# Kernel tuning notes

Measured on AMD Instinct MI355X. Metric: run time of the kernel, lower is better.

Reference implementation:

```python
import jax, jax.numpy as jnp
import numpy as np

N_NODES = 128   # input_series_dim (nodes per graph)
FEAT = 512      # input_series_length
HID = 512       # hidden_channels
OUT = 10        # output_dimension
BATCH = 512     # batch_size


def setup_inputs() -> dict:
    key = jax.random.key(0)
    ks = jax.random.split(key, 9)
    s = 0.02
    x = jax.random.normal(ks[0], (BATCH, N_NODES, FEAT), jnp.float32)
    # dense_to_sparse(ones(N_NODES, N_NODES)) -> fully connected incl. diagonal,
    # row-major order, covering only nodes 0..N_NODES-1 (faithful to source).
    r = jnp.repeat(jnp.arange(N_NODES, dtype=jnp.int32), N_NODES)
    c = jnp.tile(jnp.arange(N_NODES, dtype=jnp.int32), N_NODES)
    edge_index = jnp.stack([r, c])  # (2, N_NODES**2)
    batch = jnp.repeat(jnp.arange(BATCH, dtype=jnp.int32), N_NODES)  # (BATCH*N_NODES,)
    W1 = jax.random.normal(ks[1], (FEAT, HID), jnp.float32) * s
    b1 = jnp.zeros((HID,), jnp.float32)
    W2 = jax.random.normal(ks[2], (HID, HID), jnp.float32) * s
    b2 = jnp.zeros((HID,), jnp.float32)
    W3 = jax.random.normal(ks[3], (HID, HID), jnp.float32) * s
    b3 = jnp.zeros((HID,), jnp.float32)
    Wlin = jax.random.normal(ks[4], (HID, OUT), jnp.float32) * s
    blin = jnp.zeros((OUT,), jnp.float32)
    return {"x": x, "W1": W1, "b1": b1, "W2": W2, "b2": b2, "W3": W3,
            "b3": b3, "Wlin": Wlin, "blin": blin,
            "edge_index": edge_index, "batch": batch}


def gcn_conv(h, src, dst, W, b):
    # PyG GCNConv: linear transform, add self-loops for ALL N nodes, symmetric norm,
    # scatter-add aggregate at dst, add bias.
    N = h.shape[0]
    h = h @ W
    loop = jnp.arange(N, dtype=src.dtype)
    s = jnp.concatenate([src, loop])
    d = jnp.concatenate([dst, loop])
    deg = jax.ops.segment_sum(jnp.ones(s.shape[0], h.dtype), d, num_segments=N)
    dinv = jnp.where(deg > 0, jax.lax.rsqrt(deg), jnp.zeros((), h.dtype))
    norm = dinv[s] * dinv[d]                     # (E+N,)
    out = jax.ops.segment_sum(norm[:, None] * h[s], d, num_segments=N)
    return out + b


def reference(x, W1, b1, W2, b2, W3, b3, Wlin, blin, edge_index, batch):
    x = x.reshape(-1, x.shape[-1]).astype(jnp.float32)   # (B*N_NODES, FEAT)
    src, dst = edge_index[0], edge_index[1]
    h = jax.nn.relu(gcn_conv(x, src, dst, W1, b1))
    h = jax.nn.relu(gcn_conv(h, src, dst, W2, b2))
    h = gcn_conv(h, src, dst, W3, b3)                    # layers == 3 path
    B = BATCH
    sums = jax.ops.segment_sum(h, batch, num_segments=B)
    cnt = jax.ops.segment_sum(jnp.ones((h.shape[0],), h.dtype), batch, num_segments=B)
    pooled = sums / cnt[:, None]                         # global_mean_pool
    # dropout p=0.5 is identity in eval mode
    return pooled @ Wlin + blin                          # (BATCH, OUT)
```

## Files before the change

### kernel.cpp

```cpp
#include <hip/hip_runtime.h>
#include <hip/hip_bf16.h>


typedef __attribute__((ext_vector_type(8))) short short8;
typedef __attribute__((ext_vector_type(4))) float f32x4;
typedef __attribute__((ext_vector_type(2))) unsigned int uint2v;
typedef __attribute__((ext_vector_type(4))) unsigned int uint4v;

#define AS_G __attribute__((address_space(1)))
#define AS_L __attribute__((address_space(3)))

__device__ __forceinline__ void gload_lds16(const void* g, void* l) {
  __builtin_amdgcn_global_load_lds((const AS_G void*)g, (AS_L void*)l, 16, 0, 0);
}

__device__ __forceinline__ unsigned int pack2_bf16(float a, float b) {
  unsigned int ua = __float_as_uint(a);
  unsigned int ub = __float_as_uint(b);
  ua += 0x7FFFu + ((ua >> 16) & 1u);
  ub += 0x7FFFu + ((ub >> 16) & 1u);
  return (ua >> 16) | (ub & 0xFFFF0000u);
}

__device__ __forceinline__ unsigned short bf16_rne(float a) {
  unsigned int ua = __float_as_uint(a);
  ua += 0x7FFFu + ((ua >> 16) & 1u);
  return (unsigned short)(ua >> 16);
}

__global__ __launch_bounds__(512, 4) void gemm1(
    const float* __restrict__ x,
    const __hip_bfloat16* __restrict__ W1t,
    const float* __restrict__ b1,
    unsigned short* __restrict__ H1)
{
  __shared__ __align__(16) __hip_bfloat16 smem[26368];

  const int t    = threadIdx.x;
  const int orig = blockIdx.x;
  const int wgid = (orig & 7) * 128 + (orig >> 3);
  const int g    = wgid >> 1;
  const int nb   = wgid & 1;

  const int wave = t >> 6;
  const int l    = t & 63;
  const int q    = l >> 4;
  const int r16  = l & 15;
  const int wm   = (wave & 1) * 64;
  const int wn   = (wave >> 1) * 64;

  const int arow = t >> 2;
  const int cc   = t & 3;
  const float* gx = x + ((size_t)g * 128 + arow) * 512 + cc * 8;
  const int awoff = arow * 32 + ((cc ^ ((arow >> 1) & 3)) << 3);

  const int nrow0 = t >> 2;
  const int nrow1 = (512 + t) >> 2;
  const int slot  = t & 3;
  const __hip_bfloat16* gb0 = W1t + (size_t)(nb * 256 + nrow0) * 512 +
                              ((slot ^ ((nrow0 >> 1) & 3)) << 3);
  const __hip_bfloat16* gb1 = W1t + (size_t)(nb * 256 + nrow1) * 512 +
                              ((slot ^ ((nrow1 >> 1) & 3)) << 3);

  f32x4 acc[4][4];
#pragma unroll
  for (int i = 0; i < 4; ++i)
#pragma unroll
    for (int j = 0; j < 4; ++j)
      acc[i][j] = (f32x4)0.0f;

  {
    f32x4 a0 = *(const f32x4*)(const void*)gx;
    f32x4 a1 = *(const f32x4*)(const void*)(gx + 4);
    gload_lds16(gb0, smem + 8192 + wave * 512);
    gload_lds16(gb1, smem + 8192 + 4096 + wave * 512);
    uint4v w;
    w[0] = pack2_bf16(a0[0], a0[1]);
    w[1] = pack2_bf16(a0[2], a0[3]);
    w[2] = pack2_bf16(a1[0], a1[1]);
    w[3] = pack2_bf16(a1[2], a1[3]);
    *(uint4v*)(void*)(smem + awoff) = w;
  }

  for (int kt = 0; kt < 16; ++kt) {
    const int cur = kt & 1;
    const int nxt = cur ^ 1;
    __syncthreads();

    f32x4 aN0, aN1;
    if (kt < 15) {
      const int ko = (kt + 1) * 32;
      aN0 = *(const f32x4*)(const void*)(gx + ko);
      aN1 = *(const f32x4*)(const void*)(gx + ko + 4);
      gload_lds16(gb0 + ko, smem + 8192 + nxt * 8192 + wave * 512);
      gload_lds16(gb1 + ko, smem + 8192 + nxt * 8192 + 4096 + wave * 512);
    }

    short8 af[4], bfr[4];
#pragma unroll
    for (int i = 0; i < 4; ++i) {
      const int row = wm + i * 16 + r16;
      const int c   = (q ^ ((row >> 1) & 3)) << 3;
      af[i] = *(const short8*)(const void*)(smem + cur * 4096 + row * 32 + c);
    }
#pragma unroll
    for (int j = 0; j < 4; ++j) {
      const int row = wn + j * 16 + r16;
      const int c   = (q ^ ((row >> 1) & 3)) << 3;
      bfr[j] = *(const short8*)(const void*)(smem + 8192 + cur * 8192 + row * 32 + c);
    }
    __builtin_amdgcn_s_setprio(1);
#pragma unroll
    for (int i = 0; i < 4; ++i)
#pragma unroll
      for (int j = 0; j < 4; ++j)
        acc[i][j] = __builtin_amdgcn_mfma_f32_16x16x32_bf16(af[i], bfr[j], acc[i][j], 0, 0, 0);
    __builtin_amdgcn_s_setprio(0);

    if (kt < 15) {
      uint4v w;
      w[0] = pack2_bf16(aN0[0], aN0[1]);
      w[1] = pack2_bf16(aN0[2], aN0[3]);
      w[2] = pack2_bf16(aN1[0], aN1[1]);
      w[3] = pack2_bf16(aN1[2], aN1[3]);
      *(uint4v*)(void*)(smem + nxt * 4096 + awoff) = w;
    }
  }

  float* redf = (float*)(smem + 24576);
  float* Sbuf = (float*)(smem + 25600);

  if (g == 0) {
    float sj[4];
#pragma unroll
    for (int j = 0; j < 4; ++j) {
      float a = 0.0f;
#pragma unroll
      for (int i = 0; i < 4; ++i)
#pragma unroll
        for (int r = 0; r < 4; ++r)
          a += acc[i][j][r];
      a += __shfl_xor(a, 16, 64);
      a += __shfl_xor(a, 32, 64);
      sj[j] = a;
    }
    __syncthreads();
    if (q == 0) {
#pragma unroll
      for (int j = 0; j < 4; ++j) redf[wave * 64 + j * 16 + r16] = sj[j];
    }
    __syncthreads();
    if (t < 256)
      Sbuf[t] = redf[(2 * (t >> 6)) * 64 + (t & 63)] +
                redf[(2 * (t >> 6) + 1) * 64 + (t & 63)];
    __syncthreads();
#pragma unroll
    for (int j = 0; j < 4; ++j) {
      const int col = wn + j * 16 + r16;
      const float bv = b1[nb * 256 + col];
      const float Sv = Sbuf[col];
#pragma unroll
      for (int i = 0; i < 4; ++i)
#pragma unroll
        for (int r = 0; r < 4; ++r) {
          const int row = wm + i * 16 + q * 4 + r;
          const float v = fmaxf((Sv + acc[i][j][r]) * (1.0f / 129.0f) + bv, 0.0f);
          const float o = __shfl_xor(v, 1, 64);
          if ((r16 & 1) == 0)
            *(unsigned int*)(void*)(H1 + (size_t)(g * 128 + row) * 512 + nb * 256 + col) =
                pack2_bf16(v, o);
        }
    }
  } else {
#pragma unroll
    for (int j = 0; j < 4; ++j) {
      const int col = wn + j * 16 + r16;
      const float bv = b1[nb * 256 + col];
#pragma unroll
      for (int i = 0; i < 4; ++i)
#pragma unroll
        for (int r = 0; r < 4; ++r) {
          const int row = wm + i * 16 + q * 4 + r;
          const float v = fmaxf(acc[i][j][r] + bv, 0.0f);
          const float o = __shfl_xor(v, 1, 64);
          if ((r16 & 1) == 0)
            *(unsigned int*)(void*)(H1 + (size_t)(g * 128 + row) * 512 + nb * 256 + col) =
                pack2_bf16(v, o);
        }
    }
  }
}

__global__ __launch_bounds__(512, 4) void gemm2(
    const unsigned short* __restrict__ H1,
    const __hip_bfloat16* __restrict__ W2t,
    const float* __restrict__ b2,
    float* __restrict__ P)
{
  __shared__ __align__(16) __hip_bfloat16 smem[26368];

  const int t    = threadIdx.x;
  const int orig = blockIdx.x;
  const int wgid = (orig & 7) * 128 + (orig >> 3);
  const int g    = wgid >> 1;
  const int nb   = wgid & 1;

  const int wave = t >> 6;
  const int l    = t & 63;
  const int q    = l >> 4;
  const int r16  = l & 15;
  const int wm   = (wave & 1) * 64;
  const int wn   = (wave >> 1) * 64;

  const int arow = t >> 2;
  const int slot = t & 3;
  const unsigned short* gaA = H1 + (size_t)(g * 128 + arow) * 512 +
                              ((slot ^ ((arow >> 1) & 3)) << 3);
  const int nrow0 = t >> 2;
  const int nrow1 = (512 + t) >> 2;
  const __hip_bfloat16* gb0 = W2t + (size_t)(nb * 256 + nrow0) * 512 +
                              ((slot ^ ((nrow0 >> 1) & 3)) << 3);
  const __hip_bfloat16* gb1 = W2t + (size_t)(nb * 256 + nrow1) * 512 +
                              ((slot ^ ((nrow1 >> 1) & 3)) << 3);

  f32x4 acc[4][4];
#pragma unroll
  for (int i = 0; i < 4; ++i)
#pragma unroll
    for (int j = 0; j < 4; ++j)
      acc[i][j] = (f32x4)0.0f;

  gload_lds16(gaA, smem + wave * 512);
  gload_lds16(gb0, smem + 8192 + wave * 512);
  gload_lds16(gb1, smem + 8192 + 4096 + wave * 512);

  for (int kt = 0; kt < 16; ++kt) {
    const int cur = kt & 1;
    const int nxt = cur ^ 1;
    __syncthreads();

    if (kt < 15) {
      const int ko = (kt + 1) * 32;
      gload_lds16(gaA + ko, smem + nxt * 4096 + wave * 512);
      gload_lds16(gb0 + ko, smem + 8192 + nxt * 8192 + wave * 512);
      gload_lds16(gb1 + ko, smem + 8192 + nxt * 8192 + 4096 + wave * 512);
    }

    short8 af[4], bfr[4];
#pragma unroll
    for (int i = 0; i < 4; ++i) {
      const int row = wm + i * 16 + r16;
      const int c   = (q ^ ((row >> 1) & 3)) << 3;
      af[i] = *(const short8*)(const void*)(smem + cur * 4096 + row * 32 + c);
    }
#pragma unroll
    for (int j = 0; j < 4; ++j) {
      const int row = wn + j * 16 + r16;
      const int c   = (q ^ ((row >> 1) & 3)) << 3;
      bfr[j] = *(const short8*)(const void*)(smem + 8192 + cur * 8192 + row * 32 + c);
    }
    __builtin_amdgcn_s_setprio(1);
#pragma unroll
    for (int i = 0; i < 4; ++i)
#pragma unroll
      for (int j = 0; j < 4; ++j)
        acc[i][j] = __builtin_amdgcn_mfma_f32_16x16x32_bf16(af[i], bfr[j], acc[i][j], 0, 0, 0);
    __builtin_amdgcn_s_setprio(0);
  }

  float* redf = (float*)(smem + 24576);
  float* Sbuf = (float*)(smem + 25600);

  float pj[4];
  if (g == 0) {
    float sj[4];
#pragma unroll
    for (int j = 0; j < 4; ++j) {
      float a = 0.0f;
#pragma unroll
      for (int i = 0; i < 4; ++i)
#pragma unroll
        for (int r = 0; r < 4; ++r)
          a += acc[i][j][r];
      a += __shfl_xor(a, 16, 64);
      a += __shfl_xor(a, 32, 64);
      sj[j] = a;
    }
    __syncthreads();
    if (q == 0) {
#pragma unroll
      for (int j = 0; j < 4; ++j) redf[wave * 64 + j * 16 + r16] = sj[j];
    }
    __syncthreads();
    if (t < 256)
      Sbuf[t] = redf[(2 * (t >> 6)) * 64 + (t & 63)] +
                redf[(2 * (t >> 6) + 1) * 64 + (t & 63)];
    __syncthreads();
#pragma unroll
    for (int j = 0; j < 4; ++j) {
      const int col = wn + j * 16 + r16;
      const float bv = b2[nb * 256 + col];
      const float Sv = Sbuf[col];
      float a = 0.0f;
#pragma unroll
      for (int i = 0; i < 4; ++i)
#pragma unroll
        for (int r = 0; r < 4; ++r)
          a += fmaxf((Sv + acc[i][j][r]) * (1.0f / 129.0f) + bv, 0.0f);
      a += __shfl_xor(a, 16, 64);
      a += __shfl_xor(a, 32, 64);
      pj[j] = a;
    }
    __syncthreads();
  } else {
#pragma unroll
    for (int j = 0; j < 4; ++j) {
      const float bv = b2[nb * 256 + wn + j * 16 + r16];
      float a = 0.0f;
#pragma unroll
      for (int i = 0; i < 4; ++i)
#pragma unroll
        for (int r = 0; r < 4; ++r)
          a += fmaxf(acc[i][j][r] + bv, 0.0f);
      a += __shfl_xor(a, 16, 64);
      a += __shfl_xor(a, 32, 64);
      pj[j] = a;
    }
    __syncthreads();
  }
  if (q == 0) {
#pragma unroll
    for (int j = 0; j < 4; ++j) redf[wave * 64 + j * 16 + r16] = pj[j];
  }
  __syncthreads();
  if (t < 256)
    P[(size_t)g * 512 + nb * 256 + t] =
        (redf[(2 * (t >> 6)) * 64 + (t & 63)] +
         redf[(2 * (t >> 6) + 1) * 64 + (t & 63)]) * (1.0f / 128.0f);
}

__global__ void final_out(const float* __restrict__ P,
                          const float* __restrict__ Wf,
                          const float* __restrict__ bfv,
                          float* __restrict__ out) {
  const int m = blockIdx.x;
  const int l = threadIdx.x;
  float acc[10];
#pragma unroll
  for (int o = 0; o < 10; ++o) acc[o] = 0.0f;
  for (int c = l; c < 512; c += 64) {
    const float p = P[m * 512 + c];
#pragma unroll
    for (int o = 0; o < 10; ++o) acc[o] += p * Wf[c * 10 + o];
  }
#pragma unroll
  for (int off = 32; off; off >>= 1)
#pragma unroll
    for (int o = 0; o < 10; ++o) acc[o] += __shfl_down(acc[o], off, 64);
  if (l == 0) {
#pragma unroll
    for (int o = 0; o < 10; ++o) out[m * 10 + o] = acc[o] + bfv[o];
  }
}

__global__ __launch_bounds__(1024) void fused_gcn(
    const float* __restrict__ x,
    const __hip_bfloat16* __restrict__ W1t,
    const __hip_bfloat16* __restrict__ W2t,
    const float* __restrict__ b1,
    const float* __restrict__ b2,
    const float* __restrict__ Wf,
    const float* __restrict__ bfv,
    float* __restrict__ out)
{
  __shared__ __align__(16) __hip_bfloat16 smem[81920];

  const int t  = threadIdx.x;
  const int g  = blockIdx.x;
  const int wave = t >> 6;
  const int l    = t & 63;
  const int q    = l >> 4;
  const int r16  = l & 15;
  const int wm   = (wave & 1) * 64;
  const int wn   = (wave >> 1) * 64;

  const int arow = t >> 3;
  const int kq   = t & 7;
  const float* ga = x + ((size_t)g * 128 + arow) * 512 + kq * 4;
  const int awoff = arow * 32 + (((kq >> 1) ^ ((arow >> 1) & 3)) << 3) + (kq & 1) * 4;

  const int brow = t >> 2;
  const int bgc  = (t & 3) ^ ((brow >> 1) & 3);
  const size_t boff = (size_t)brow * 512 + bgc * 8;
  const __hip_bfloat16* g1b0 = W1t + boff;
  const __hip_bfloat16* g1b1 = g1b0 + (size_t)256 * 512;

  f32x4 acc[4][4];
#pragma unroll
  for (int i = 0; i < 4; ++i)
#pragma unroll
    for (int j = 0; j < 4; ++j)
      acc[i][j] = (f32x4)0.0f;

  {
    f32x4 a0 = *(const f32x4*)(const void*)ga;
    gload_lds16(g1b0, smem + 49152 + wave * 512);
    gload_lds16(g1b1, smem + 49152 + 8192 + wave * 512);
    uint2v w;
    w[0] = pack2_bf16(a0[0], a0[1]);
    w[1] = pack2_bf16(a0[2], a0[3]);
    *(uint2v*)(void*)(smem + awoff) = w;
  }
  for (int kt = 0; kt < 16; ++kt) {
    const int cur = kt & 1;
    const int nxt = cur ^ 1;
    __syncthreads();

    f32x4 aN;
    if (kt < 15) {
      const int ko = (kt + 1) * 32;
      aN = *(const f32x4*)(const void*)(ga + ko);
      gload_lds16(g1b0 + ko, smem + 49152 + nxt * 16384 + wave * 512);
      gload_lds16(g1b1 + ko, smem + 49152 + nxt * 16384 + 8192 + wave * 512);
    }

    short8 af[4], bfr[4];
#pragma unroll
    for (int i = 0; i < 4; ++i) {
      const int row = wm + i * 16 + r16;
      const int c   = (q ^ ((row >> 1) & 3)) << 3;
      af[i] = *(const short8*)(const void*)(smem + cur * 4096 + row * 32 + c);
    }
#pragma unroll
    for (int j = 0; j < 4; ++j) {
      const int row = wn + j * 16 + r16;
      const int c   = (q ^ ((row >> 1) & 3)) << 3;
      bfr[j] = *(const short8*)(const void*)(smem + 49152 + cur * 16384 + row * 32 + c);
    }
#pragma unroll
    for (int i = 0; i < 4; ++i)
#pragma unroll
      for (int j = 0; j < 4; ++j)
        acc[i][j] = __builtin_amdgcn_mfma_f32_16x16x32_bf16(af[i], bfr[j], acc[i][j], 0, 0, 0);

    if (kt < 15) {
      uint2v w;
      w[0] = pack2_bf16(aN[0], aN[1]);
      w[1] = pack2_bf16(aN[2], aN[3]);
      *(uint2v*)(void*)(smem + nxt * 4096 + awoff) = w;
    }
  }
  __syncthreads();

  const __hip_bfloat16* g2b0 = W2t + boff;
  const __hip_bfloat16* g2b1 = g2b0 + (size_t)256 * 512;
  gload_lds16(g2b0, smem + 65536 + wave * 512);

  float* redf = (float*)(smem + 73728);
  float* Sbuf = (float*)(smem + 75776);

  if (g == 0) {
    float sj[4];
#pragma unroll
    for (int j = 0; j < 4; ++j) {
      float a = 0.0f;
#pragma unroll
      for (int i = 0; i < 4; ++i)
#pragma unroll
        for (int r = 0; r < 4; ++r)
          a += acc[i][j][r];
      a += __shfl_xor(a, 16, 64);
      a += __shfl_xor(a, 32, 64);
      sj[j] = a;
    }
    if (q == 0) {
#pragma unroll
      for (int j = 0; j < 4; ++j) redf[wave * 64 + j * 16 + r16] = sj[j];
    }
    __syncthreads();
    if (t < 512)
      Sbuf[t] = redf[((t >> 6) * 2) * 64 + (t & 63)] +
                redf[((t >> 6) * 2 + 1) * 64 + (t & 63)];
    __syncthreads();
#pragma unroll
    for (int j = 0; j < 4; ++j) {
      const int col = wn + j * 16 + r16;
      const float bv = b1[col];
      const float Sv = Sbuf[col];
#pragma unroll
      for (int i = 0; i < 4; ++i)
#pragma unroll
        for (int r = 0; r < 4; ++r) {
          const int row = wm + i * 16 + q * 4 + r;
          const float v = fmaxf((Sv + acc[i][j][r]) * (1.0f / 129.0f) + bv, 0.0f);
          const float o = __shfl_xor(v, 1, 64);
          if ((r16 & 1) == 0) {
            const int sl = (col >> 3) ^ (row & 7);
            *(unsigned int*)(void*)(smem + row * 512 + sl * 8 + (col & 7)) = pack2_bf16(v, o);
          }
        }
    }
  } else {
#pragma unroll
    for (int j = 0; j < 4; ++j) {
      const int col = wn + j * 16 + r16;
      const float bv = b1[col];
#pragma unroll
      for (int i = 0; i < 4; ++i)
#pragma unroll
        for (int r = 0; r < 4; ++r) {
          const int row = wm + i * 16 + q * 4 + r;
          const float v = fmaxf(acc[i][j][r] + bv, 0.0f);
          const float o = __shfl_xor(v, 1, 64);
          if ((r16 & 1) == 0) {
            const int sl = (col >> 3) ^ (row & 7);
            *(unsigned int*)(void*)(smem + row * 512 + sl * 8 + (col & 7)) = pack2_bf16(v, o);
          }
        }
    }
  }

#pragma unroll
  for (int i = 0; i < 4; ++i)
#pragma unroll
    for (int j = 0; j < 4; ++j)
      acc[i][j] = (f32x4)0.0f;

  for (int kt = 0; kt < 16; ++kt) {
    __syncthreads();
    gload_lds16(g2b1 + kt * 32, smem + 73728 + wave * 512);
    if (wave < 8) {
      short8 af[4], bfr[4];
#pragma unroll
      for (int i = 0; i < 4; ++i) {
        const int row = wm + i * 16 + r16;
        const int sl  = (kt * 4 + q) ^ (row & 7);
        af[i] = *(const short8*)(const void*)(smem + row * 512 + sl * 8);
      }
#pragma unroll
      for (int j = 0; j < 4; ++j) {
        const int row = wn + j * 16 + r16;
        const int c   = (q ^ ((row >> 1) & 3)) << 3;
        bfr[j] = *(const short8*)(const void*)(smem + 65536 + row * 32 + c);
      }
      __builtin_amdgcn_s_setprio(1);
#pragma unroll
      for (int i = 0; i < 4; ++i)
#pragma unroll
        for (int j = 0; j < 4; ++j)
          acc[i][j] = __builtin_amdgcn_mfma_f32_16x16x32_bf16(af[i], bfr[j], acc[i][j], 0, 0, 0);
      __builtin_amdgcn_s_setprio(0);
    }
    __syncthreads();
    if (kt < 15)
      gload_lds16(g2b0 + (kt + 1) * 32, smem + 65536 + wave * 512);
    if (wave >= 8) {
      short8 af[4], bfr[4];
#pragma unroll
      for (int i = 0; i < 4; ++i) {
        const int row = wm + i * 16 + r16;
        const int sl  = (kt * 4 + q) ^ (row & 7);
        af[i] = *(const short8*)(const void*)(smem + row * 512 + sl * 8);
      }
#pragma unroll
      for (int j = 0; j < 4; ++j) {
        const int row = wn + j * 16 + r16;
        const int c   = (q ^ ((row >> 1) & 3)) << 3;
        bfr[j] = *(const short8*)(const void*)(smem + 65536 + row * 32 + c);
      }
      __builtin_amdgcn_s_setprio(1);
#pragma unroll
      for (int i = 0; i < 4; ++i)
#pragma unroll
        for (int j = 0; j < 4; ++j)
          acc[i][j] = __builtin_amdgcn_mfma_f32_16x16x32_bf16(af[i], bfr[j], acc[i][j], 0, 0, 0);
      __builtin_amdgcn_s_setprio(0);
    }
  }
  __syncthreads();

  float pj[4];
  if (g == 0) {
    float sj[4];
#pragma unroll
    for (int j = 0; j < 4; ++j) {
      float a = 0.0f;
#pragma unroll
      for (int i = 0; i < 4; ++i)
#pragma unroll
        for (int r = 0; r < 4; ++r)
          a += acc[i][j][r];
      a += __shfl_xor(a, 16, 64);
      a += __shfl_xor(a, 32, 64);
      sj[j] = a;
    }
    if (q == 0) {
#pragma unroll
      for (int j = 0; j < 4; ++j) redf[wave * 64 + j * 16 + r16] = sj[j];
    }
    __syncthreads();
    if (t < 512)
      Sbuf[t] = redf[((t >> 6) * 2) * 64 + (t & 63)] +
                redf[((t >> 6) * 2 + 1) * 64 + (t & 63)];
    __syncthreads();
#pragma unroll
    for (int j = 0; j < 4; ++j) {
      const float bv = b2[wn + j * 16 + r16];
      const float Sv = Sbuf[wn + j * 16 + r16];
      float a = 0.0f;
#pragma unroll
      for (int i = 0; i < 4; ++i)
#pragma unroll
        for (int r = 0; r < 4; ++r)
          a += fmaxf((Sv + acc[i][j][r]) * (1.0f / 129.0f) + bv, 0.0f);
      a += __shfl_xor(a, 16, 64);
      a += __shfl_xor(a, 32, 64);
      pj[j] = a;
    }
  } else {
#pragma unroll
    for (int j = 0; j < 4; ++j) {
      const float bv = b2[wn + j * 16 + r16];
      float a = 0.0f;
#pragma unroll
      for (int i = 0; i < 4; ++i)
#pragma unroll
        for (int r = 0; r < 4; ++r)
          a += fmaxf(acc[i][j][r] + bv, 0.0f);
      a += __shfl_xor(a, 16, 64);
      a += __shfl_xor(a, 32, 64);
      pj[j] = a;
    }
  }
  if (q == 0) {
#pragma unroll
    for (int j = 0; j < 4; ++j) redf[wave * 64 + j * 16 + r16] = pj[j];
  }
  __syncthreads();
  if (t < 512)
    Sbuf[t] =
        (redf[((t >> 6) * 2) * 64 + (t & 63)] +
         redf[((t >> 6) * 2 + 1) * 64 + (t & 63)]) * (1.0f / 128.0f);
  __syncthreads();

  if (wave < 10) {
    float s = 0.0f;
    for (int c = l; c < 512; c += 64) s += Sbuf[c] * Wf[c * 10 + wave];
#pragma unroll
    for (int off = 32; off; off >>= 1) s += __shfl_down(s, off, 64);
    if (l == 0) out[(size_t)g * 10 + wave] = s + bfv[wave];
  }
}

__global__ __launch_bounds__(1024) void prep(
    const float* __restrict__ W1, const float* __restrict__ W2,
    unsigned short* __restrict__ W1t, unsigned short* __restrict__ W2t,
    const float* __restrict__ W3, const float* __restrict__ Wlin,
    const float* __restrict__ b3, const float* __restrict__ blin,
    float* __restrict__ Wf, float* __restrict__ bfv) {
  const int b = blockIdx.x;
  if (b < 512) {
    __shared__ float tile[32][33];
    const int z  = b >> 8;
    const int by = (b >> 4) & 15;
    const int bx = b & 15;
    const float* W = z ? W2 : W1;
    unsigned short* Wt = z ? W2t : W1t;
    const int tx = threadIdx.x & 31;
    const int ty = threadIdx.x >> 5;
    tile[ty][tx] = W[(by * 32 + ty) * 512 + bx * 32 + tx];
    __syncthreads();
    Wt[(bx * 32 + ty) * 512 + by * 32 + tx] = bf16_rne(tile[tx][ty]);
  } else {
    const int c = b - 512;
    const int l = threadIdx.x;
    if (l < 64) {
      float acc[10];
#pragma unroll
      for (int o = 0; o < 10; ++o) acc[o] = 0.0f;
      for (int n = l; n < 512; n += 64) {
        const float wv = W3[c * 512 + n];
#pragma unroll
        for (int o = 0; o < 10; ++o) acc[o] += wv * Wlin[n * 10 + o];
      }
#pragma unroll
      for (int off = 32; off; off >>= 1)
#pragma unroll
        for (int o = 0; o < 10; ++o) acc[o] += __shfl_down(acc[o], off, 64);
      if (l == 0) {
#pragma unroll
        for (int o = 0; o < 10; ++o) Wf[c * 10 + o] = acc[o];
      }
      if (c < 10) {
        float s = 0.0f;
        for (int k = l; k < 512; k += 64) s += b3[k] * Wlin[k * 10 + c];
#pragma unroll
        for (int off = 32; off; off >>= 1) s += __shfl_down(s, off, 64);
        if (l == 0) bfv[c] = s + blin[c];
      }
    }
  }
}

extern "C" void kernel_launch(void* const* d_in, const int* in_sizes, int n_in,
                              void* d_out, int out_size, void* d_ws, size_t ws_size,
                              hipStream_t stream) {
  const float* x    = (const float*)d_in[0];
  const float* W1   = (const float*)d_in[1];
  const float* b1   = (const float*)d_in[2];
  const float* W2   = (const float*)d_in[3];
  const float* b2   = (const float*)d_in[4];
  const float* W3   = (const float*)d_in[5];
  const float* b3   = (const float*)d_in[6];
  const float* Wlin = (const float*)d_in[7];
  const float* blin = (const float*)d_in[8];
  float* out = (float*)d_out;

  char* ws = (char*)d_ws;
  unsigned short* W1t = (unsigned short*)ws;
  unsigned short* W2t = W1t + 512 * 512;
  float* Wf           = (float*)(W2t + 512 * 512);
  float* bfv          = Wf + 512 * 10;
  float* P            = bfv + 16;
  unsigned short* H1  = (unsigned short*)(P + 512 * 512);

  const size_t need = (size_t)(W2t + 512 * 512 - W1t) * 2 +
                      (512 * 10 + 16 + 512 * 512) * 4 +
                      (size_t)65536 * 512 * 2;

  prep<<<1024, 1024, 0, stream>>>(W1, W2, W1t, W2t, W3, Wlin, b3, blin, Wf, bfv);

  if (ws_size >= need) {
    gemm1<<<1024, 512, 0, stream>>>(
        x, (const __hip_bfloat16*)W1t, b1, H1);
    gemm2<<<1024, 512, 0, stream>>>(
        H1, (const __hip_bfloat16*)W2t, b2, P);
    final_out<<<512, 64, 0, stream>>>(P, Wf, bfv, out);
  } else {
    fused_gcn<<<512, 1024, 0, stream>>>(
        x, (const __hip_bfloat16*)W1t, (const __hip_bfloat16*)W2t, b1, b2, Wf, bfv, out);
  }
}
```

Baseline: 320.8 us.

## Pre-convert x to bf16 in prep and stream it via global_load_lds in gemm1

Adds a pass to the prep kernel that converts the fp32 input x into a bf16 copy in the workspace. gemm1 then loads its A operand straight into LDS with global_load_lds instead of reading fp32 into registers, packing it, and writing it to LDS. The goal is to take the register round trip and conversion out of the GEMM main loop. In exchange the full 128MB x is read and 64MB is written and re-read, which adds HBM traffic. The epilogue loops are also reordered and bias loads hoisted.

Measured after the change: 297.2 us. 7.3% less time.

```diff
diff --git a/kernel.cpp b/kernel.cpp
--- a/kernel.cpp
+++ b/kernel.cpp
@@ -5,7 +5,6 @@
 typedef __attribute__((ext_vector_type(8))) short short8;
 typedef __attribute__((ext_vector_type(4))) float f32x4;
 typedef __attribute__((ext_vector_type(2))) unsigned int uint2v;
-typedef __attribute__((ext_vector_type(4))) unsigned int uint4v;
 
 #define AS_G __attribute__((address_space(1)))
 #define AS_L __attribute__((address_space(3)))
@@ -29,7 +28,7 @@
 }
 
 __global__ __launch_bounds__(512, 4) void gemm1(
-    const float* __restrict__ x,
+    const unsigned short* __restrict__ xb,
     const __hip_bfloat16* __restrict__ W1t,
     const float* __restrict__ b1,
     unsigned short* __restrict__ H1)
@@ -50,13 +49,11 @@
   const int wn   = (wave >> 1) * 64;
 
   const int arow = t >> 2;
-  const int cc   = t & 3;
-  const float* gx = x + ((size_t)g * 128 + arow) * 512 + cc * 8;
-  const int awoff = arow * 32 + ((cc ^ ((arow >> 1) & 3)) << 3);
-
+  const int slot = t & 3;
+  const unsigned short* gaA = xb + (size_t)(g * 128 + arow) * 512 +
+                              ((slot ^ ((arow >> 1) & 3)) << 3);
   const int nrow0 = t >> 2;
-  const int nrow1 = (512 + t) >> 2;
-  const int slot  = t & 3;
+  const int nrow1 = 128 + (t >> 2);
   const __hip_bfloat16* gb0 = W1t + (size_t)(nb * 256 + nrow0) * 512 +
                               ((slot ^ ((nrow0 >> 1) & 3)) << 3);
   const __hip_bfloat16* gb1 = W1t + (size_t)(nb * 256 + nrow1) * 512 +
@@ -69,29 +66,18 @@
     for (int j = 0; j < 4; ++j)
       acc[i][j] = (f32x4)0.0f;
 
-  {
-    f32x4 a0 = *(const f32x4*)(const void*)gx;
-    f32x4 a1 = *(const f32x4*)(const void*)(gx + 4);
-    gload_lds16(gb0, smem + 8192 + wave * 512);
-    gload_lds16(gb1, smem + 8192 + 4096 + wave * 512);
-    uint4v w;
-    w[0] = pack2_bf16(a0[0], a0[1]);
-    w[1] = pack2_bf16(a0[2], a0[3]);
-    w[2] = pack2_bf16(a1[0], a1[1]);
-    w[3] = pack2_bf16(a1[2], a1[3]);
-    *(uint4v*)(void*)(smem + awoff) = w;
-  }
+  gload_lds16(gaA, smem + wave * 512);
+  gload_lds16(gb0, smem + 8192 + wave * 512);
+  gload_lds16(gb1, smem + 8192 + 4096 + wave * 512);
 
   for (int kt = 0; kt < 16; ++kt) {
     const int cur = kt & 1;
     const int nxt = cur ^ 1;
     __syncthreads();
 
-    f32x4 aN0, aN1;
     if (kt < 15) {
       const int ko = (kt + 1) * 32;
-      aN0 = *(const f32x4*)(const void*)(gx + ko);
-      aN1 = *(const f32x4*)(const void*)(gx + ko + 4);
+      gload_lds16(gaA + ko, smem + nxt * 4096 + wave * 512);
       gload_lds16(gb0 + ko, smem + 8192 + nxt * 8192 + wave * 512);
       gload_lds16(gb1 + ko, smem + 8192 + nxt * 8192 + 4096 + wave * 512);
     }
@@ -116,19 +102,11 @@
       for (int j = 0; j < 4; ++j)
         acc[i][j] = __builtin_amdgcn_mfma_f32_16x16x32_bf16(af[i], bfr[j], acc[i][j], 0, 0, 0);
     __builtin_amdgcn_s_setprio(0);
-
-    if (kt < 15) {
-      uint4v w;
-      w[0] = pack2_bf16(aN0[0], aN0[1]);
-      w[1] = pack2_bf16(aN0[2], aN0[3]);
-      w[2] = pack2_bf16(aN1[0], aN1[1]);
-      w[3] = pack2_bf16(aN1[2], aN1[3]);
-      *(uint4v*)(void*)(smem + nxt * 4096 + awoff) = w;
-    }
   }
 
   float* redf = (float*)(smem + 24576);
   float* Sbuf = (float*)(smem + 25600);
+  const size_t hbase = (size_t)g * 128 * 512 + nb * 256;
 
   if (g == 0) {
     float sj[4];
@@ -154,40 +132,44 @@
       Sbuf[t] = redf[(2 * (t >> 6)) * 64 + (t & 63)] +
                 redf[(2 * (t >> 6) + 1) * 64 + (t & 63)];
     __syncthreads();
-#pragma unroll
-    for (int j = 0; j < 4; ++j) {
-      const int col = wn + j * 16 + r16;
-      const float bv = b1[nb * 256 + col];
-      const float Sv = Sbuf[col];
-#pragma unroll
-      for (int i = 0; i < 4; ++i)
-#pragma unroll
-        for (int r = 0; r < 4; ++r) {
-          const int row = wm + i * 16 + q * 4 + r;
-          const float v = fmaxf((Sv + acc[i][j][r]) * (1.0f / 129.0f) + bv, 0.0f);
+    float bvv[4], Svv[4];
+#pragma unroll
+    for (int j = 0; j < 4; ++j) {
+      bvv[j] = b1[nb * 256 + wn + j * 16 + r16];
+      Svv[j] = Sbuf[wn + j * 16 + r16];
+    }
+#pragma unroll
+    for (int i = 0; i < 4; ++i)
+#pragma unroll
+      for (int r = 0; r < 4; ++r) {
+        const int row = wm + i * 16 + q * 4 + r;
+#pragma unroll
+        for (int j = 0; j < 4; ++j) {
+          const float v = fmaxf((Svv[j] + acc[i][j][r]) * (1.0f / 129.0f) + bvv[j], 0.0f);
           const float o = __shfl_xor(v, 1, 64);
           if ((r16 & 1) == 0)
-            *(unsigned int*)(void*)(H1 + (size_t)(g * 128 + row) * 512 + nb * 256 + col) =
+            *(unsigned int*)(void*)(H1 + hbase + (size_t)row * 512 + wn + j * 16 + r16) =
                 pack2_bf16(v, o);
         }
-    }
+      }
   } else {
-#pragma unroll
-    for (int j = 0; j < 4; ++j) {
-      const int col = wn + j * 16 + r16;
-      const float bv = b1[nb * 256 + col];
-#pragma unroll
-      for (int i = 0; i < 4; ++i)
-#pragma unroll
-        for (int r = 0; r < 4; ++r) {
-          const int row = wm + i * 16 + q * 4 + r;
-          const float v = fmaxf(acc[i][j][r] + bv, 0.0f);
+    float bvv[4];
+#pragma unroll
+    for (int j = 0; j < 4; ++j) bvv[j] = b1[nb * 256 + wn + j * 16 + r16];
+#pragma unroll
+    for (int i = 0; i < 4; ++i)
+#pragma unroll
+      for (int r = 0; r < 4; ++r) {
+        const int row = wm + i * 16 + q * 4 + r;
+#pragma unroll
+        for (int j = 0; j < 4; ++j) {
+          const float v = fmaxf(acc[i][j][r] + bvv[j], 0.0f);
           const float o = __shfl_xor(v, 1, 64);
           if ((r16 & 1) == 0)
-            *(unsigned int*)(void*)(H1 + (size_t)(g * 128 + row) * 512 + nb * 256 + col) =
+            *(unsigned int*)(void*)(H1 + hbase + (size_t)row * 512 + wn + j * 16 + r16) =
                 pack2_bf16(v, o);
         }
-    }
+      }
   }
 }
 
@@ -217,7 +199,7 @@
   const unsigned short* gaA = H1 + (size_t)(g * 128 + arow) * 512 +
                               ((slot ^ ((arow >> 1) & 3)) << 3);
   const int nrow0 = t >> 2;
-  const int nrow1 = (512 + t) >> 2;
+  const int nrow1 = 128 + (t >> 2);
   const __hip_bfloat16* gb0 = W2t + (size_t)(nb * 256 + nrow0) * 512 +
                               ((slot ^ ((nrow0 >> 1) & 3)) << 3);
   const __hip_bfloat16* gb1 = W2t + (size_t)(nb * 256 + nrow1) * 512 +
@@ -657,7 +639,8 @@
     unsigned short* __restrict__ W1t, unsigned short* __restrict__ W2t,
     const float* __restrict__ W3, const float* __restrict__ Wlin,
     const float* __restrict__ b3, const float* __restrict__ blin,
-    float* __restrict__ Wf, float* __restrict__ bfv) {
+    float* __restrict__ Wf, float* __restrict__ bfv,
+    const float* __restrict__ x, unsigned short* __restrict__ xb) {
   const int b = blockIdx.x;
   if (b < 512) {
     __shared__ float tile[32][33];
@@ -671,7 +654,7 @@
     tile[ty][tx] = W[(by * 32 + ty) * 512 + bx * 32 + tx];
     __syncthreads();
     Wt[(bx * 32 + ty) * 512 + by * 32 + tx] = bf16_rne(tile[tx][ty]);
-  } else {
+  } else if (b < 1024) {
     const int c = b - 512;
     const int l = threadIdx.x;
     if (l < 64) {
@@ -698,6 +681,18 @@
         for (int off = 32; off; off >>= 1) s += __shfl_down(s, off, 64);
         if (l == 0) bfv[c] = s + blin[c];
       }
+    }
+  } else {
+    const size_t base = (size_t)(b - 1024) * 8192;
+    const int tt = threadIdx.x;
+#pragma unroll
+    for (int jj = 0; jj < 2; ++jj) {
+      const size_t off = base + (size_t)jj * 4096 + (size_t)tt * 4;
+      const f32x4 v = *(const f32x4*)(const void*)(x + off);
+      uint2v w;
+      w[0] = pack2_bf16(v[0], v[1]);
+      w[1] = pack2_bf16(v[2], v[3]);
+      *(uint2v*)(void*)(xb + off) = w;
     }
   }
 }
@@ -723,18 +718,20 @@
   float* bfv          = Wf + 512 * 10;
   float* P            = bfv + 16;
   unsigned short* H1  = (unsigned short*)(P + 512 * 512);
-
-  const size_t need = (size_t)(W2t + 512 * 512 - W1t) * 2 +
+  unsigned short* xb  = H1 + (size_t)65536 * 512;
+
+  const size_t need = (size_t)512 * 512 * 2 * 2 +
                       (512 * 10 + 16 + 512 * 512) * 4 +
-                      (size_t)65536 * 512 * 2;
-
-  prep<<<1024, 1024, 0, stream>>>(W1, W2, W1t, W2t, W3, Wlin, b3, blin, Wf, bfv);
-
-  if (ws_size >= need) {
-    gemm1<<<1024, 512, 0, stream>>>(
-        x, (const __hip_bfloat16*)W1t, b1, H1);
-    gemm2<<<1024, 512, 0, stream>>>(
-        H1, (const __hip_bfloat16*)W2t, b2, P);
+                      (size_t)65536 * 512 * 2 * 2;
+
+  const bool split = ws_size >= need;
+
+  prep<<<split ? 5120 : 1024, 1024, 0, stream>>>(
+      W1, W2, W1t, W2t, W3, Wlin, b3, blin, Wf, bfv, x, xb);
+
+  if (split) {
+    gemm1<<<1024, 512, 0, stream>>>(xb, (const __hip_bfloat16*)W1t, b1, H1);
+    gemm2<<<1024, 512, 0, stream>>>(H1, (const __hip_bfloat16*)W2t, b2, P);
     final_out<<<512, 64, 0, stream>>>(P, Wf, bfv, out);
   } else {
     fused_gcn<<<512, 1024, 0, stream>>>(
```
